# Optimization experiments

Measured on AMD Instinct MI355X. Metric: run time of the kernel, lower is better.

## Reference

```python
import jax, jax.numpy as jnp
import numpy as np

NUM_HEADS = 12
ALPHA = 0.5
TANH_CLIP = 5.0


def setup_inputs() -> dict:
    key = jax.random.key(0)
    k1, k2, k3, k4, k5 = jax.random.split(key, 5)
    B, N, C = 8, 1024, 768
    x = jax.random.normal(k1, (B, N, C), dtype=jnp.float32)
    # qkv: Linear(C -> 3C), proj: Linear(C -> C); torch stores weight as [out, in]
    s = 1.0 / np.sqrt(C)
    qkv_w = jax.random.normal(k2, (3 * C, C), dtype=jnp.float32) * s
    qkv_b = jax.random.normal(k3, (3 * C,), dtype=jnp.float32) * 0.02
    proj_w = jax.random.normal(k4, (C, C), dtype=jnp.float32) * s
    proj_b = jax.random.normal(k5, (C,), dtype=jnp.float32) * 0.02
    return {"x": x, "qkv_w": qkv_w, "qkv_b": qkv_b, "proj_w": proj_w, "proj_b": proj_b}


def reference(x, qkv_w, qkv_b, proj_w, proj_b):
    B, N, C = x.shape
    H = NUM_HEADS
    D = C // H
    scale = D ** -0.5
    # qkv projection -> [B, N, 3, H, D] -> q/k/v each [B, H, N, D]
    qkv = (x @ qkv_w.T + qkv_b).reshape(B, N, 3, H, D)
    qkv = jnp.transpose(qkv, (2, 0, 3, 1, 4))
    q, k, v = qkv[0], qkv[1], qkv[2]
    # pre-softmax scores [B, H, N, N]
    scores = jnp.einsum("bhnd,bhmd->bhnm", q * scale, k)
    scores_t = jnp.swapaxes(scores, -2, -1)
    scores_sym = 0.5 * (scores + scores_t)
    scores_asym = 0.5 * (scores - scores_t)
    scores = scores_sym + ALPHA * scores_asym
    # gamma_mode == 'approx'
    gamma = np.sqrt((1.0 + ALPHA ** 2) / 2.0)
    scores = scores / gamma
    # tanh clip
    scores = TANH_CLIP * jnp.tanh(scores / TANH_CLIP)
    attn = jax.nn.softmax(scores, axis=-1)
    out = jnp.einsum("bhnm,bhmd->bhnd", attn, v)  # [B, H, N, D]
    out = jnp.transpose(out, (0, 2, 1, 3)).reshape(B, N, C)
    return out @ proj_w.T + proj_b
```

## Files before the change

kernel.cpp:

```cpp
#include <hip/hip_runtime.h>
#include <hip/hip_bf16.h>
#include <stdint.h>

typedef unsigned short u16;
typedef __attribute__((ext_vector_type(8))) short bf16x8;
typedef __attribute__((ext_vector_type(4))) float f32x4;

#define LDS_AS(p) ((__attribute__((address_space(3))) void*)(p))
#define GLB_AS(p) ((__attribute__((address_space(1))) void*)(p))

__device__ __forceinline__ u16 f2bf(float f) {
  union { float f; uint32_t u; } v; v.f = f;
  uint32_t u = v.u;
  u += 0x7fffu + ((u >> 16) & 1u);
  return (u16)(u >> 16);
}

__device__ __forceinline__ float exp2_fast(float x) {
  float r;
  asm("v_exp_f32 %0, %1" : "=v"(r) : "v"(x));
  return r;
}

__device__ __forceinline__ float bits2f(uint32_t u) {
  union { uint32_t u; float f; } v; v.u = u; return v.f;
}
__device__ __forceinline__ uint32_t f2bits(float f) {
  union { float f; uint32_t u; } v; v.f = f; return v.u;
}
__device__ __forceinline__ uint32_t pack_hi16(uint32_t lo_src, uint32_t hi_src) {
  return __builtin_amdgcn_perm(hi_src, lo_src, 0x07060302u);
}

__device__ __forceinline__ void cvt8(const float* __restrict__ s, u16* __restrict__ d) {
  const float4* sv = (const float4*)s;
  float4 a = sv[0], b = sv[1];
  uint4 o;
  o.x = (uint32_t)f2bf(a.x) | ((uint32_t)f2bf(a.y) << 16);
  o.y = (uint32_t)f2bf(a.z) | ((uint32_t)f2bf(a.w) << 16);
  o.z = (uint32_t)f2bf(b.x) | ((uint32_t)f2bf(b.y) << 16);
  o.w = (uint32_t)f2bf(b.z) | ((uint32_t)f2bf(b.w) << 16);
  *(uint4*)d = o;
}

__global__ __launch_bounds__(256) void k_convert(
    const float* __restrict__ x, const float* __restrict__ wq, const float* __restrict__ wp,
    u16* __restrict__ xb, u16* __restrict__ wqb, u16* __restrict__ wpb) {
  int tid = blockIdx.x * 256 + threadIdx.x;
  int np  = gridDim.x * 256;
  for (int i = tid; i < (8192*768)/8; i += np) cvt8(x  + (size_t)i*8, xb  + (size_t)i*8);
  for (int i = tid; i < (2304*768)/8; i += np) cvt8(wq + (size_t)i*8, wqb + (size_t)i*8);
  for (int i = tid; i < (768*768)/8;  i += np) cvt8(wp + (size_t)i*8, wpb + (size_t)i*8);
}

template<bool SWAP>
__device__ __forceinline__ void gemm_core(const u16* __restrict__ A,
                                          const u16* __restrict__ B,
                                          u16* As, u16* Bs,
                                          int rowA0, int rowB0,
                                          f32x4 acc[4][4]) {
  const int t  = threadIdx.x;
  const int lane = t & 63;
  const int wv = t >> 6;
  const int wr = wv >> 1, wc = wv & 1;
  const int lr = lane & 15, lg = lane >> 4;

#define GSTAGE(KT, BUF)                                                                         \
  {                                                                                             \
    _Pragma("unroll")                                                                           \
    for (int p = 0; p < 2; ++p) {                                                               \
      int idx = p * 256 + t;                                                                    \
      int row = idx >> 2;                                                                       \
      int cc  = (idx & 3) ^ ((row >> 1) & 3);                                                   \
      __builtin_amdgcn_global_load_lds(GLB_AS(A + (size_t)(rowA0 + row) * 768 + (KT) * 32 + cc * 8), \
                                       LDS_AS(As + (BUF) * 4096 + idx * 8), 16, 0, 0);          \
    }                                                                                           \
    _Pragma("unroll")                                                                           \
    for (int p = 0; p < 2; ++p) {                                                               \
      int idx = p * 256 + t;                                                                    \
      int row = idx >> 2;                                                                       \
      int cc  = (idx & 3) ^ ((row >> 1) & 3);                                                   \
      __builtin_amdgcn_global_load_lds(GLB_AS(B + (size_t)(rowB0 + row) * 768 + (KT) * 32 + cc * 8), \
                                       LDS_AS(Bs + (BUF) * 4096 + idx * 8), 16, 0, 0);          \
    }                                                                                           \
  }

  GSTAGE(0, 0);

#pragma unroll 1
  for (int kt = 0; kt < 24; ++kt) {
    const int cur = kt & 1;
    __syncthreads();

    if (kt < 23) GSTAGE(kt + 1, cur ^ 1);

    const u16* Ab = As + cur * 4096;
    const u16* Bb = Bs + cur * 4096;
    bf16x8 af[4], bf_[4];
#pragma unroll
    for (int mi = 0; mi < 4; ++mi) {
      int row = wr * 64 + mi * 16 + lr;
      int cc  = lg ^ ((row >> 1) & 3);
      af[mi] = *(const bf16x8*)(Ab + row * 32 + cc * 8);
    }
#pragma unroll
    for (int ni = 0; ni < 4; ++ni) {
      int row = wc * 64 + ni * 16 + lr;
      int cc  = lg ^ ((row >> 1) & 3);
      bf_[ni] = *(const bf16x8*)(Bb + row * 32 + cc * 8);
    }
#pragma unroll
    for (int mi = 0; mi < 4; ++mi)
#pragma unroll
      for (int ni = 0; ni < 4; ++ni) {
        if (SWAP)
          acc[mi][ni] = __builtin_amdgcn_mfma_f32_16x16x32_bf16(bf_[ni], af[mi], acc[mi][ni], 0, 0, 0);
        else
          acc[mi][ni] = __builtin_amdgcn_mfma_f32_16x16x32_bf16(af[mi], bf_[ni], acc[mi][ni], 0, 0, 0);
      }
  }
#undef GSTAGE
}

__global__ __launch_bounds__(256) void k_gemm_qkv(
    const u16* __restrict__ Aq, const u16* __restrict__ Bw, const float* __restrict__ bias,
    u16* __restrict__ Qh, u16* __restrict__ Kh, u16* __restrict__ Vt) {
  __shared__ u16 As[2 * 128 * 32];
  __shared__ u16 Bs[2 * 128 * 32];
  int bid = blockIdx.x;
  int wg  = (bid & 7) * 144 + (bid >> 3);
  int bx  = wg % 18, by = wg / 18;

  const int t = threadIdx.x, lane = t & 63, wv = t >> 6;
  const int wr = wv >> 1, wc = wv & 1, lr = lane & 15, lg = lane >> 4;
  const int tsec = bx / 6;
  const int colBase = bx * 128 + wc * 64;

  const float gam = 0.7905694150420949f;
  const float rC1 = __builtin_sqrtf(0.57707801636f);
  const float sc1 = __builtin_sqrtf(0.09375f / gam) * rC1;
  const float sc2 = __builtin_sqrtf(0.03125f / gam) * rC1;

  f32x4 acc[4][4];
#pragma unroll
  for (int mi = 0; mi < 4; ++mi)
#pragma unroll
    for (int ni = 0; ni < 4; ++ni) acc[mi][ni] = (f32x4){0.f, 0.f, 0.f, 0.f};

  if (tsec < 2) {
    gemm_core<true>(Aq, Bw, As, Bs, by * 128, bx * 128, acc);

    float4 bv4[4];
#pragma unroll
    for (int ni = 0; ni < 4; ++ni)
      bv4[ni] = *(const float4*)(bias + colBase + ni * 16 + lg * 4);

#pragma unroll
    for (int mi = 0; mi < 4; ++mi) {
      int n = by * 128 + wr * 64 + mi * 16 + lr;
      int b = n >> 10, nn = n & 1023;
#pragma unroll
      for (int ni = 0; ni < 4; ++ni) {
        int fs = colBase - tsec * 768 + ni * 16 + lg * 4;
        int h = fs >> 6, d = fs & 63;
        size_t rowq = ((size_t)(b * 12 + h) * 1024 + nn) * 128;
        float v0 = acc[mi][ni][0] + bv4[ni].x;
        float v1 = acc[mi][ni][1] + bv4[ni].y;
        float v2 = acc[mi][ni][2] + bv4[ni].z;
        float v3 = acc[mi][ni][3] + bv4[ni].w;
        uint2 wq_, wk_;
        wq_.x = (uint32_t)f2bf(v0 * sc1) | ((uint32_t)f2bf(v1 * sc1) << 16);
        wq_.y = (uint32_t)f2bf(v2 * sc1) | ((uint32_t)f2bf(v3 * sc1) << 16);
        wk_.x = (uint32_t)f2bf(v0 * sc2) | ((uint32_t)f2bf(v1 * sc2) << 16);
        wk_.y = (uint32_t)f2bf(v2 * sc2) | ((uint32_t)f2bf(v3 * sc2) << 16);
        if (tsec == 0) {
          *(uint2*)(Qh + rowq + d)      = wq_;
          *(uint2*)(Kh + rowq + 64 + d) = wk_;
        } else {
          *(uint2*)(Kh + rowq + d)      = wq_;
          *(uint2*)(Qh + rowq + 64 + d) = wk_;
        }
      }
    }
  } else {
    gemm_core<false>(Aq, Bw, As, Bs, by * 128, bx * 128, acc);

    float bv[4];
#pragma unroll
    for (int ni = 0; ni < 4; ++ni) bv[ni] = bias[colBase + ni * 16 + lr];

#pragma unroll
    for (int mi = 0; mi < 4; ++mi) {
      int tok0 = by * 128 + wr * 64 + mi * 16 + lg * 4;
      int b = tok0 >> 10, n0 = tok0 & 1023;
#pragma unroll
      for (int ni = 0; ni < 4; ++ni) {
        int fs = colBase - 2 * 768 + ni * 16 + lr;
        int h = fs >> 6, d = fs & 63;
        float v0 = acc[mi][ni][0] + bv[ni];
        float v1 = acc[mi][ni][1] + bv[ni];
        float v2 = acc[mi][ni][2] + bv[ni];
        float v3 = acc[mi][ni][3] + bv[ni];
        uint2 w;
        w.x = (uint32_t)f2bf(v0) | ((uint32_t)f2bf(v1) << 16);
        w.y = (uint32_t)f2bf(v2) | ((uint32_t)f2bf(v3) << 16);
        *(uint2*)(Vt + ((size_t)((b * 12 + h) * 64 + d)) * 1024 + n0) = w;
      }
    }
  }
}

__global__ __launch_bounds__(256, 3) void k_attn(
    const u16* __restrict__ Qh, const u16* __restrict__ Kh, const u16* __restrict__ Vt,
    u16* __restrict__ attn) {
  __shared__ u16 Ks[3][32 * 128];
  __shared__ u16 Vs[3][64 * 32];
  __shared__ u16 Ps[4][32 * 40];

  int bid = blockIdx.x;
  int wg = (bid & 7) * 96 + (bid >> 3);
  int bh = wg >> 3, qb = wg & 7;
  int b = bh / 12, h = bh % 12;

  const int t = threadIdx.x, lane = t & 63, wv = t >> 6;
  const int lr = lane & 15, lg = lane >> 4;

  const size_t khb = (size_t)bh * 1024 * 128;
  const size_t vtb = (size_t)bh * 64 * 1024;

  bf16x8 qf[2][4];
  {
    const u16* qp = Qh + ((size_t)bh * 1024 + qb * 128 + wv * 32 + lr) * 128 + lg * 8;
#pragma unroll
    for (int it = 0; it < 2; ++it)
#pragma unroll
      for (int kk = 0; kk < 4; ++kk)
        qf[it][kk] = *(const bf16x8*)(qp + it * 16 * 128 + kk * 32);
  }
  asm volatile("s_waitcnt vmcnt(0)" ::: "memory");
  __builtin_amdgcn_sched_barrier(0);

#define STAGE(KT, BUF)                                                                         \
  {                                                                                            \
    _Pragma("unroll")                                                                          \
    for (int p = 0; p < 2; ++p) {                                                              \
      int idx = p * 256 + t;                                                                   \
      int row = idx >> 4;                                                                      \
      int cc  = (idx & 15) ^ (row & 7);                                                        \
      __builtin_amdgcn_global_load_lds(GLB_AS(Kh + khb + (size_t)((KT) * 32 + row) * 128 + cc * 8), \
                                       LDS_AS(Ks[BUF] + idx * 8), 16, 0, 0);                   \
    }                                                                                          \
    {                                                                                          \
      int d = t >> 2;                                                                          \
      int g = (t & 3) ^ ((d + (d >> 2)) & 3);                                                  \
      __builtin_amdgcn_global_load_lds(GLB_AS(Vt + vtb + (size_t)d * 1024 + (KT) * 32 + g * 8),\
                                       LDS_AS(Vs[BUF] + t * 8), 16, 0, 0);                     \
    }                                                                                          \
  }

  STAGE(0, 0);
  STAGE(1, 1);

  f32x4 acc_o[4][2];
#pragma unroll
  for (int dt = 0; dt < 4; ++dt)
#pragma unroll
    for (int it = 0; it < 2; ++it) acc_o[dt][it] = (f32x4){0.f, 0.f, 0.f, 0.f};
  float dsum[2] = {0.f, 0.f};

  u16* pw = Ps[wv];
  const float C2 = -14.4269504089f;

  int cur = 0, stg = 2;
#pragma unroll 1
  for (int kt = 0; kt < 32; ++kt) {
    if (kt < 31) {
      asm volatile("s_waitcnt vmcnt(3)" ::: "memory");
    } else {
      asm volatile("s_waitcnt vmcnt(0)" ::: "memory");
    }
    __builtin_amdgcn_sched_barrier(0);
    __builtin_amdgcn_s_barrier();
    __builtin_amdgcn_sched_barrier(0);

    if (kt < 30) STAGE(kt + 2, stg);

    const u16* K0 = Ks[cur];
    f32x4 accs[2][2];
#pragma unroll
    for (int jt = 0; jt < 2; ++jt)
#pragma unroll
      for (int it = 0; it < 2; ++it) accs[jt][it] = (f32x4){0.f, 0.f, 0.f, 0.f};
    __builtin_amdgcn_s_setprio(1);
#pragma unroll
    for (int jt = 0; jt < 2; ++jt) {
#pragma unroll
      for (int kk = 0; kk < 4; ++kk) {
        int row = jt * 16 + lr;
        int cc  = (kk * 4 + lg) ^ (row & 7);
        bf16x8 kf = *(const bf16x8*)(K0 + row * 128 + cc * 8);
#pragma unroll
        for (int it = 0; it < 2; ++it)
          accs[jt][it] = __builtin_amdgcn_mfma_f32_16x16x32_bf16(kf, qf[it][kk], accs[jt][it], 0, 0, 0);
      }
    }
    __builtin_amdgcn_s_setprio(0);

#pragma unroll
    for (int jt = 0; jt < 2; ++jt) {
#pragma unroll
      for (int it = 0; it < 2; ++it) {
        float p0 = exp2_fast(C2 * __builtin_amdgcn_rcpf(exp2_fast(accs[jt][it][0]) + 1.0f));
        float p1 = exp2_fast(C2 * __builtin_amdgcn_rcpf(exp2_fast(accs[jt][it][1]) + 1.0f));
        float p2 = exp2_fast(C2 * __builtin_amdgcn_rcpf(exp2_fast(accs[jt][it][2]) + 1.0f));
        float p3 = exp2_fast(C2 * __builtin_amdgcn_rcpf(exp2_fast(accs[jt][it][3]) + 1.0f));
        uint32_t a0 = f2bits(p0), a1 = f2bits(p1), a2 = f2bits(p2), a3 = f2bits(p3);
        uint2 w;
        w.x = pack_hi16(a0, a1);
        w.y = pack_hi16(a2, a3);
        dsum[it] += (bits2f(a0 & 0xFFFF0000u) + bits2f(a1 & 0xFFFF0000u))
                  + (bits2f(a2 & 0xFFFF0000u) + bits2f(a3 & 0xFFFF0000u));
        *(uint2*)(pw + (it * 16 + lr) * 40 + jt * 16 + lg * 4) = w;
      }
    }

    asm volatile("" ::: "memory");

    {
      const u16* V0 = Vs[cur];
      bf16x8 pa[2];
#pragma unroll
      for (int it = 0; it < 2; ++it)
        pa[it] = *(const bf16x8*)(pw + (it * 16 + lr) * 40 + lg * 8);
      __builtin_amdgcn_s_setprio(1);
#pragma unroll
      for (int dt = 0; dt < 4; ++dt) {
        int row = dt * 16 + lr;
        int ph  = lg ^ ((row + (row >> 2)) & 3);
        bf16x8 vf = *(const bf16x8*)(V0 + row * 32 + ph * 8);
#pragma unroll
        for (int it = 0; it < 2; ++it)
          acc_o[dt][it] = __builtin_amdgcn_mfma_f32_16x16x32_bf16(vf, pa[it], acc_o[dt][it], 0, 0, 0);
      }
      __builtin_amdgcn_s_setprio(0);
    }

    cur = (cur == 2) ? 0 : cur + 1;
    stg = (stg == 2) ? 0 : stg + 1;
  }
#undef STAGE

  float rinv[2];
#pragma unroll
  for (int it = 0; it < 2; ++it) {
    float v = dsum[it];
    v += __shfl_xor(v, 16);
    v += __shfl_xor(v, 32);
    rinv[it] = __builtin_amdgcn_rcpf(v);
  }

#pragma unroll
  for (int dt = 0; dt < 4; ++dt) {
#pragma unroll
    for (int it = 0; it < 2; ++it) {
      float v0 = acc_o[dt][it][0] * rinv[it];
      float v1 = acc_o[dt][it][1] * rinv[it];
      float v2 = acc_o[dt][it][2] * rinv[it];
      float v3 = acc_o[dt][it][3] * rinv[it];
      uint2 w;
      w.x = (uint32_t)f2bf(v0) | ((uint32_t)f2bf(v1) << 16);
      w.y = (uint32_t)f2bf(v2) | ((uint32_t)f2bf(v3) << 16);
      int n = qb * 128 + wv * 32 + it * 16 + lr;
      *(uint2*)(attn + ((size_t)(b * 1024 + n)) * 768 + h * 64 + dt * 16 + lg * 4) = w;
    }
  }
}

__global__ __launch_bounds__(256) void k_gemm_proj(
    const u16* __restrict__ Ain, const u16* __restrict__ Bw, const float* __restrict__ bias,
    float* __restrict__ out) {
  __shared__ u16 As[2 * 128 * 32];
  __shared__ u16 Bs[2 * 128 * 32];
  int bid = blockIdx.x;
  int wg  = (bid & 7) * 48 + (bid >> 3);
  int bx  = wg % 6, by = wg / 6;

  f32x4 acc[4][4];
#pragma unroll
  for (int mi = 0; mi < 4; ++mi)
#pragma unroll
    for (int ni = 0; ni < 4; ++ni) acc[mi][ni] = (f32x4){0.f, 0.f, 0.f, 0.f};

  gemm_core<false>(Ain, Bw, As, Bs, by * 128, bx * 128, acc);

  const int t = threadIdx.x, lane = t & 63, wv = t >> 6;
  const int wr = wv >> 1, wc = wv & 1, lr = lane & 15, lg = lane >> 4;
  const int col0 = bx * 128 + wc * 64;

  float bv[4];
#pragma unroll
  for (int ni = 0; ni < 4; ++ni) bv[ni] = bias[col0 + ni * 16 + lr];

#pragma unroll
  for (int mi = 0; mi < 4; ++mi) {
    int tok0 = by * 128 + wr * 64 + mi * 16 + lg * 4;
#pragma unroll
    for (int ni = 0; ni < 4; ++ni) {
      int col = col0 + ni * 16 + lr;
#pragma unroll
      for (int r = 0; r < 4; ++r) {
        out[(size_t)(tok0 + r) * 768 + col] = acc[mi][ni][r] + bv[ni];
      }
    }
  }
}

extern "C" void kernel_launch(void* const* d_in, const int* in_sizes, int n_in,
                              void* d_out, int out_size, void* d_ws, size_t ws_size,
                              hipStream_t stream) {
  (void)in_sizes; (void)n_in; (void)out_size;
  const float* x      = (const float*)d_in[0];
  const float* qkv_w  = (const float*)d_in[1];
  const float* qkv_b  = (const float*)d_in[2];
  const float* proj_w = (const float*)d_in[3];
  const float* proj_b = (const float*)d_in[4];
  float* out = (float*)d_out;

  uint8_t* ws = (uint8_t*)d_ws;
  u16* xb  = (u16*)(ws + 0);
  u16* wqb = (u16*)(ws + 12582912);
  u16* wpb = (u16*)(ws + 16121856);
  u16* Qh  = (u16*)(ws + 17301504);
  u16* Kh  = (u16*)(ws + 42467328);
  u16* Vt  = (u16*)(ws + 80216064);
  if (ws_size < 92798976) return;

  u16* attnb = xb;

  k_convert<<<1024, 256, 0, stream>>>(x, qkv_w, proj_w, xb, wqb, wpb);
  k_gemm_qkv<<<1152, 256, 0, stream>>>(xb, wqb, qkv_b, Qh, Kh, Vt);
  k_attn<<<768, 256, 0, stream>>>(Qh, Kh, Vt, attnb);
  k_gemm_proj<<<384, 256, 0, stream>>>(attnb, wpb, proj_b, out);
}
```

Baseline: 150.0 us.

## Use 64-key tiles with single K buffer and double-buffered V staging

Switches the attention loop from 32-key tiles with a 3-deep K/V ring to 64-key tiles. K now has a single LDS buffer that is refilled right after the QK MFMAs, with an extra barrier. V is double-buffered and loaded one tile ahead. This halves the number of loop iterations and barriers and gives more MFMA work per iteration. In exchange the K load is exposed behind only the softmax and PV phase, and the explicit vmcnt-based waits are replaced by plain __syncthreads.

```diff
diff --git a/kernel.cpp b/kernel.cpp
--- a/kernel.cpp
+++ b/kernel.cpp
@@ -213,9 +213,9 @@
 __global__ __launch_bounds__(256, 3) void k_attn(
     const u16* __restrict__ Qh, const u16* __restrict__ Kh, const u16* __restrict__ Vt,
     u16* __restrict__ attn) {
-  __shared__ u16 Ks[3][32 * 128];
-  __shared__ u16 Vs[3][64 * 32];
-  __shared__ u16 Ps[4][32 * 40];
+  __shared__ u16 Ks[64 * 128];
+  __shared__ u16 Vs[2][64 * 64];
+  __shared__ u16 Ps[4][2][32 * 40];
 
   int bid = blockIdx.x;
   int wg = (bid & 7) * 96 + (bid >> 3);
@@ -237,29 +237,32 @@
       for (int kk = 0; kk < 4; ++kk)
         qf[it][kk] = *(const bf16x8*)(qp + it * 16 * 128 + kk * 32);
   }
-  asm volatile("s_waitcnt vmcnt(0)" ::: "memory");
-  __builtin_amdgcn_sched_barrier(0);
-
-#define STAGE(KT, BUF)                                                                         \
+
+#define STAGE_K(KT)                                                                            \
+  {                                                                                            \
+    _Pragma("unroll")                                                                          \
+    for (int p = 0; p < 4; ++p) {                                                              \
+      int idx = p * 256 + t;                                                                   \
+      int row = idx >> 4;                                                                      \
+      int cc  = (idx & 15) ^ (row & 7);                                                        \
+      __builtin_amdgcn_global_load_lds(GLB_AS(Kh + khb + (size_t)((KT) * 64 + row) * 128 + cc * 8), \
+                                       LDS_AS(Ks + idx * 8), 16, 0, 0);                        \
+    }                                                                                          \
+  }
+#define STAGE_V(KT, BUF)                                                                       \
   {                                                                                            \
     _Pragma("unroll")                                                                          \
     for (int p = 0; p < 2; ++p) {                                                              \
       int idx = p * 256 + t;                                                                   \
-      int row = idx >> 4;                                                                      \
-      int cc  = (idx & 15) ^ (row & 7);                                                        \
-      __builtin_amdgcn_global_load_lds(GLB_AS(Kh + khb + (size_t)((KT) * 32 + row) * 128 + cc * 8), \
-                                       LDS_AS(Ks[BUF] + idx * 8), 16, 0, 0);                   \
+      int d   = idx >> 3;                                                                      \
+      int g   = (idx & 7) ^ (d & 7);                                                           \
+      __builtin_amdgcn_global_load_lds(GLB_AS(Vt + vtb + (size_t)d * 1024 + (KT) * 64 + g * 8),\
+                                       LDS_AS(Vs[BUF] + idx * 8), 16, 0, 0);                   \
     }                                                                                          \
-    {                                                                                          \
-      int d = t >> 2;                                                                          \
-      int g = (t & 3) ^ ((d + (d >> 2)) & 3);                                                  \
-      __builtin_amdgcn_global_load_lds(GLB_AS(Vt + vtb + (size_t)d * 1024 + (KT) * 32 + g * 8),\
-                                       LDS_AS(Vs[BUF] + t * 8), 16, 0, 0);                     \
-    }                                                                                          \
-  }
-
-  STAGE(0, 0);
-  STAGE(1, 1);
+  }
+
+  STAGE_V(0, 0);
+  STAGE_K(0);
 
   f32x4 acc_o[4][2];
 #pragma unroll
@@ -268,37 +271,28 @@
     for (int it = 0; it < 2; ++it) acc_o[dt][it] = (f32x4){0.f, 0.f, 0.f, 0.f};
   float dsum[2] = {0.f, 0.f};
 
-  u16* pw = Ps[wv];
   const float C2 = -14.4269504089f;
 
-  int cur = 0, stg = 2;
 #pragma unroll 1
-  for (int kt = 0; kt < 32; ++kt) {
-    if (kt < 31) {
-      asm volatile("s_waitcnt vmcnt(3)" ::: "memory");
-    } else {
-      asm volatile("s_waitcnt vmcnt(0)" ::: "memory");
-    }
-    __builtin_amdgcn_sched_barrier(0);
-    __builtin_amdgcn_s_barrier();
-    __builtin_amdgcn_sched_barrier(0);
-
-    if (kt < 30) STAGE(kt + 2, stg);
-
-    const u16* K0 = Ks[cur];
-    f32x4 accs[2][2];
-#pragma unroll
-    for (int jt = 0; jt < 2; ++jt)
+  for (int kt = 0; kt < 16; ++kt) {
+    const int cur = kt & 1;
+    __syncthreads();
+
+    if (kt < 15) STAGE_V(kt + 1, cur ^ 1);
+
+    f32x4 accs[4][2];
+#pragma unroll
+    for (int jt = 0; jt < 4; ++jt)
 #pragma unroll
       for (int it = 0; it < 2; ++it) accs[jt][it] = (f32x4){0.f, 0.f, 0.f, 0.f};
     __builtin_amdgcn_s_setprio(1);
 #pragma unroll
-    for (int jt = 0; jt < 2; ++jt) {
+    for (int jt = 0; jt < 4; ++jt) {
 #pragma unroll
       for (int kk = 0; kk < 4; ++kk) {
         int row = jt * 16 + lr;
         int cc  = (kk * 4 + lg) ^ (row & 7);
-        bf16x8 kf = *(const bf16x8*)(K0 + row * 128 + cc * 8);
+        bf16x8 kf = *(const bf16x8*)(Ks + row * 128 + cc * 8);
 #pragma unroll
         for (int it = 0; it < 2; ++it)
           accs[jt][it] = __builtin_amdgcn_mfma_f32_16x16x32_bf16(kf, qf[it][kk], accs[jt][it], 0, 0, 0);
@@ -306,8 +300,12 @@
     }
     __builtin_amdgcn_s_setprio(0);
 
-#pragma unroll
-    for (int jt = 0; jt < 2; ++jt) {
+    __syncthreads();
+    if (kt < 15) STAGE_K(kt + 1);
+
+#pragma unroll
+    for (int jt = 0; jt < 4; ++jt) {
+      const int ks = jt >> 1, jtl = jt & 1;
 #pragma unroll
       for (int it = 0; it < 2; ++it) {
         float p0 = exp2_fast(C2 * __builtin_amdgcn_rcpf(exp2_fast(accs[jt][it][0]) + 1.0f));
@@ -320,7 +318,7 @@
         w.y = pack_hi16(a2, a3);
         dsum[it] += (bits2f(a0 & 0xFFFF0000u) + bits2f(a1 & 0xFFFF0000u))
                   + (bits2f(a2 & 0xFFFF0000u) + bits2f(a3 & 0xFFFF0000u));
-        *(uint2*)(pw + (it * 16 + lr) * 40 + jt * 16 + lg * 4) = w;
+        *(uint2*)(&Ps[wv][ks][(it * 16 + lr) * 40 + jtl * 16 + lg * 4]) = w;
       }
     }
 
@@ -328,27 +326,28 @@
 
     {
       const u16* V0 = Vs[cur];
-      bf16x8 pa[2];
-#pragma unroll
-      for (int it = 0; it < 2; ++it)
-        pa[it] = *(const bf16x8*)(pw + (it * 16 + lr) * 40 + lg * 8);
-      __builtin_amdgcn_s_setprio(1);
-#pragma unroll
-      for (int dt = 0; dt < 4; ++dt) {
-        int row = dt * 16 + lr;
-        int ph  = lg ^ ((row + (row >> 2)) & 3);
-        bf16x8 vf = *(const bf16x8*)(V0 + row * 32 + ph * 8);
+#pragma unroll
+      for (int ks = 0; ks < 2; ++ks) {
+        bf16x8 pa[2];
 #pragma unroll
         for (int it = 0; it < 2; ++it)
-          acc_o[dt][it] = __builtin_amdgcn_mfma_f32_16x16x32_bf16(vf, pa[it], acc_o[dt][it], 0, 0, 0);
-      }
-      __builtin_amdgcn_s_setprio(0);
-    }
-
-    cur = (cur == 2) ? 0 : cur + 1;
-    stg = (stg == 2) ? 0 : stg + 1;
-  }
-#undef STAGE
+          pa[it] = *(const bf16x8*)(&Ps[wv][ks][(it * 16 + lr) * 40 + lg * 8]);
+        __builtin_amdgcn_s_setprio(1);
+#pragma unroll
+        for (int dt = 0; dt < 4; ++dt) {
+          int row  = dt * 16 + lr;
+          int slot = (ks * 4 + lg) ^ (lr & 7);
+          bf16x8 vf = *(const bf16x8*)(V0 + row * 64 + slot * 8);
+#pragma unroll
+          for (int it = 0; it < 2; ++it)
+            acc_o[dt][it] = __builtin_amdgcn_mfma_f32_16x16x32_bf16(vf, pa[it], acc_o[dt][it], 0, 0, 0);
+        }
+        __builtin_amdgcn_s_setprio(0);
+      }
+    }
+  }
+#undef STAGE_K
+#undef STAGE_V
 
   float rinv[2];
 #pragma unroll
```

Result: faster. 143.6 us (-4.3%).
